# Performance work log

Hardware: AMD Instinct MI355X
Metric: run time of the kernel (lower is better)

Reference implementation:

```python
import jax, jax.numpy as jnp
import numpy as np

EPS = 1e-5

def layernorm(x):
    mu = jnp.mean(x, axis=-1, keepdims=True)
    var = jnp.var(x, axis=-1, keepdims=True)
    return (x - mu) * jax.lax.rsqrt(var + EPS)

def jagged_to_padded(values, offsets, n):
    # values: [T, D]; offsets: [B+1]; -> [B, n, D] zero-padded
    lengths = offsets[1:] - offsets[:-1]            # [B]
    pos = jnp.arange(n)                             # [n]
    idx = offsets[:-1, None] + pos[None, :]         # [B, n]
    mask = pos[None, :] < lengths[:, None]          # [B, n]
    idx = jnp.clip(idx, 0, values.shape[0] - 1)
    return values[idx] * mask[..., None].astype(values.dtype)

def dense_to_jagged(padded, offsets, total):
    t = jnp.arange(total)
    b = jnp.searchsorted(offsets, t, side='right') - 1   # row of each token
    p = t - offsets[b]                                   # position within row
    return padded[b, p]

def causal_conv(x, w, b):
    # x: [B, n, D]; w: [D, D, 3]; residual + bias + leaky_relu
    xt = jnp.transpose(x, (0, 2, 1))                     # [B, D, n]
    xt = jnp.pad(xt, ((0, 0), (0, 0), (2, 0)))           # causal left pad (k-1)
    y = jax.lax.conv_general_dilated(xt, w, (1,), 'VALID',
                                     dimension_numbers=('NCH', 'OIH', 'NCH'))
    y = y + b[None, :, None]
    y = jnp.transpose(y, (0, 2, 1)) + x                  # residual
    return jax.nn.leaky_relu(y, 0.01)

def setup_inputs() -> dict:
    key = jax.random.key(0)
    ks = jax.random.split(key, 8)
    B, n, D = 32, 4096, 256
    P, H, dA = 512, 8, 64
    T = B * (n // 2)  # equal lengths of 2048
    offsets = (jnp.arange(B + 1, dtype=jnp.int64 if jax.config.read('jax_enable_x64') else jnp.int32) * (n // 2)).astype(jnp.int32)
    return {
        'normed_x': jax.random.normal(ks[0], (T, D), dtype=jnp.float32),
        'conv_w': 0.02 * jax.random.normal(ks[1], (D, D, 3), dtype=jnp.float32),
        'conv_b': 0.02 * jax.random.normal(ks[2], (D,), dtype=jnp.float32),
        'pattern': 0.02 * jax.random.normal(ks[3], (P, D), dtype=jnp.float32),
        'wq': 0.02 * jax.random.normal(ks[4], (H * dA, D), dtype=jnp.float32),
        'wkv': 0.02 * jax.random.normal(ks[5], (2 * H * dA, D), dtype=jnp.float32),
        'wout': jax.random.uniform(ks[6], (D, H * dA), dtype=jnp.float32,
                                   minval=-1.0, maxval=1.0) * np.sqrt(6.0 / (D + H * dA)),
        'bout': jnp.zeros((D,), dtype=jnp.float32),
        'x_offsets': offsets,
        'n': n,
    }

def reference(normed_x, conv_w, conv_b, pattern, wq, wkv, wout, bout, x_offsets, n):
    H, dA = 8, 64
    scale = dA ** (-0.5)
    T = normed_x.shape[0]
    # jagged -> padded, causal conv (residual + leaky_relu), padded -> jagged
    padded = jagged_to_padded(normed_x, x_offsets, n)        # [B, n, D]
    padded = causal_conv(padded, conv_w, conv_b)
    x = dense_to_jagged(padded, x_offsets, T)                # [T, D]
    # pattern layernormed twice (SPRM.forward then xattn.forward)
    pat = layernorm(layernorm(pattern))                      # [P, D]
    x = layernorm(x)
    q = (x @ wq.T).reshape(T, H, dA)                         # [T, H, dA]
    kv = (pat @ wkv.T).reshape(pat.shape[0], H, 2 * dA)
    k, v = kv[..., :dA], kv[..., dA:]                        # [P, H, dA]
    scores = scale * jnp.einsum('nhd,whd->nhw', q, k)        # [T, H, P]
    attn = jax.nn.softmax(scores, axis=-1)
    out = jnp.einsum('nhw,whd->nhd', attn, v).reshape(T, H * dA)
    out = out @ wout.T + bout                                # [T, D]
    return layernorm(out)
```

## Files before the change

### kernel.cpp

```cpp
#include <hip/hip_runtime.h>
#include <hip/hip_bf16.h>
#include <math.h>


#define EPSF 1e-5f

typedef short  s16x8 __attribute__((ext_vector_type(8)));
typedef short  s16x4 __attribute__((ext_vector_type(4)));
typedef float  f32x4 __attribute__((ext_vector_type(4)));

__device__ __forceinline__ unsigned short f2bf(float f) {
    union { float f; unsigned u; } v; v.f = f;
    unsigned r = (v.u + 0x7fffu + ((v.u >> 16) & 1u)) >> 16;
    return (unsigned short)r;
}
__device__ __forceinline__ float bf2f(unsigned short h) {
    union { unsigned u; float f; } v; v.u = ((unsigned)h) << 16;
    return v.f;
}
__device__ __forceinline__ unsigned fbits(float f) {
    union { float f; unsigned u; } v; v.f = f; return v.u;
}
__device__ __forceinline__ unsigned pk_hi(float lo, float hi) {
    return __builtin_amdgcn_perm(fbits(hi), fbits(lo), 0x07060302u);
}
__device__ __forceinline__ int inv32(int t) {
    return (t & ~31) | ((t & 0x0C) << 1) | ((t & 0x10) >> 2) | (t & 3);
}

union Bfrag { unsigned u[4]; s16x8 s; };

__global__ void cvt_kernel(const float* __restrict__ wq,
                           const float* __restrict__ wout,
                           const float* __restrict__ cw,
                           short* __restrict__ wq_bf,
                           short* __restrict__ wout_bf,
                           short* __restrict__ wck) {
    const int b = blockIdx.x, tid = threadIdx.x;
    if (b < 128) {
        const int i = (b * 256 + tid) * 4;
        const int R = i >> 8, C = i & 255;
        const float4 x = *(const float4*)(wq + i);
        s16x4 o; o[0] = f2bf(x.x); o[1] = f2bf(x.y); o[2] = f2bf(x.z); o[3] = f2bf(x.w);
        const int off = ((R >> 6) * 32 + ((R >> 4) & 3) * 8 + (C >> 5)) * 512
                      + ((R & 15) + ((C >> 3) & 3) * 16) * 8 + (C & 7);
        *(s16x4*)(wq_bf + off) = o;
    } else if (b < 256) {
        const int i = ((b - 128) * 256 + tid) * 4;
        const float4 x = *(const float4*)(wout + i);
        s16x4 o; o[0] = f2bf(x.x); o[1] = f2bf(x.y); o[2] = f2bf(x.z); o[3] = f2bf(x.w);
        *(s16x4*)(wout_bf + i) = o;
    } else {
        const int idx = (b - 256) * 256 + tid;
        const float* p = cw + (size_t)idx * 3;
        wck[idx]              = (short)f2bf(p[0]);
        wck[65536 + idx]      = (short)f2bf(p[1]);
        wck[131072 + idx]     = (short)f2bf(p[2]);
    }
}

__global__ void pat_ln_kernel(const float* __restrict__ pattern,
                              float* __restrict__ pat2) {
    __shared__ float scr[4];
    const int w = blockIdx.x;
    const int tid = threadIdx.x;
    const int lane = tid & 63, wav = tid >> 6;

    float v = pattern[(size_t)w * 256 + tid];

    float s = v;
    #pragma unroll
    for (int off = 32; off; off >>= 1) s += __shfl_xor(s, off);
    if (lane == 0) scr[wav] = s;
    __syncthreads();
    float mu = (scr[0] + scr[1] + scr[2] + scr[3]) * (1.f / 256.f);
    __syncthreads();
    float d = v - mu;
    float s2 = d * d;
    #pragma unroll
    for (int off = 32; off; off >>= 1) s2 += __shfl_xor(s2, off);
    if (lane == 0) scr[wav] = s2;
    __syncthreads();
    float var = (scr[0] + scr[1] + scr[2] + scr[3]) * (1.f / 256.f);
    float x1 = d * rsqrtf(var + EPSF);
    __syncthreads();

    s = x1;
    #pragma unroll
    for (int off = 32; off; off >>= 1) s += __shfl_xor(s, off);
    if (lane == 0) scr[wav] = s;
    __syncthreads();
    mu = (scr[0] + scr[1] + scr[2] + scr[3]) * (1.f / 256.f);
    __syncthreads();
    d = x1 - mu;
    s2 = d * d;
    #pragma unroll
    for (int off = 32; off; off >>= 1) s2 += __shfl_xor(s2, off);
    if (lane == 0) scr[wav] = s2;
    __syncthreads();
    var = (scr[0] + scr[1] + scr[2] + scr[3]) * (1.f / 256.f);
    pat2[(size_t)w * 256 + tid] = d * rsqrtf(var + EPSF);
}

__global__ __launch_bounds__(256, 2)
void kv_frag_kernel(const float* __restrict__ pat2,
                    const float* __restrict__ wkv,
                    short* __restrict__ k_bf,
                    short* __restrict__ v_t) {
    __shared__ __align__(16) float spat[32][260];
    __shared__ __align__(16) float kvs[32][65];
    const int kt = blockIdx.x, h = blockIdx.y, z = blockIdx.z;
    const int t = threadIdx.x;

    {
        const int row = t >> 3;
        const float* src = pat2 + (size_t)(kt * 32 + row) * 256 + (t & 7) * 32;
        float* dst = &spat[row][(t & 7) * 32];
        #pragma unroll
        for (int q = 0; q < 8; q++)
            *(float4*)(dst + q * 4) = *(const float4*)(src + q * 4);
    }
    __syncthreads();

    {
        const int pr = t >> 3, rb = t & 7;
        const float* srow = &spat[pr][0];
        const float* wbase = wkv + (size_t)(h * 128 + z * 64 + rb) * 256;
        float acc[8] = {0.f, 0.f, 0.f, 0.f, 0.f, 0.f, 0.f, 0.f};
        for (int i4 = 0; i4 < 64; i4++) {
            const float4 x4 = *(const float4*)(srow + i4 * 4);
            #pragma unroll
            for (int i = 0; i < 8; i++) {
                const float4 w4 = *(const float4*)(wbase + (size_t)i * 8 * 256 + i4 * 4);
                acc[i] += w4.x * x4.x + w4.y * x4.y + w4.z * x4.z + w4.w * x4.w;
            }
        }
        #pragma unroll
        for (int i = 0; i < 8; i++)
            kvs[pr][rb + 8 * i] = acc[i];
    }
    __syncthreads();

    const int lane = t & 63;
    const int cl = lane & 15, gq = lane >> 4;
    if (z == 0) {
        const int f = t >> 6;
        const int pl = ((f >> 1) << 4) | cl;
        s16x8 o;
        #pragma unroll
        for (int e = 0; e < 8; e++) {
            const int c = (f & 1) * 32 + gq * 8 + e;
            const int r = (c & ~0x1C) | ((c & 0x18) >> 1) | ((c & 4) << 2);
            o[e] = (short)f2bf(kvs[pl][r] * 0.125f);
        }
        *(s16x8*)(k_bf + (size_t)h * 32768 + (size_t)kt * 2048 + t * 8) = o;
    } else {
        const int nd = t >> 6;
        const int rd = nd * 16 + cl;
        s16x8 o;
        #pragma unroll
        for (int e = 0; e < 8; e++) {
            const int c5 = gq * 8 + e;
            const int pl = (c5 & 3) | ((c5 & 0x18) >> 1) | ((c5 & 4) << 2);
            o[e] = (short)f2bf(kvs[pl][rd]);
        }
        *(s16x8*)(v_t + (size_t)h * 32768 + (size_t)kt * 2048 + t * 8) = o;
    }
}

__global__ __launch_bounds__(256, 4)
void conv_ln_kernel(const float* __restrict__ x,
                    const short* __restrict__ wck,
                    const float* __restrict__ cb,
                    short* __restrict__ xn_bf) {
    __shared__ __align__(16) short xs[66 * 268];
    const int tid = threadIdx.x;
    const int r0 = blockIdx.x * 64;
    const int pos0 = r0 & 2047;

    #pragma unroll
    for (int it = 0; it < 17; it++) {
        const int idx = tid + it * 256;
        if (idx < 4224) {
            const int row = idx >> 6, c4 = idx & 63;
            float4 v = {0.f, 0.f, 0.f, 0.f};
            if (pos0 - 2 + row >= 0)
                v = *(const float4*)(x + (size_t)(r0 - 2 + row) * 256 + c4 * 4);
            s16x4 o; o[0] = f2bf(v.x); o[1] = f2bf(v.y); o[2] = f2bf(v.z); o[3] = f2bf(v.w);
            *(s16x4*)(xs + row * 268 + c4 * 4) = o;
        }
    }
    __syncthreads();

    const int lane = tid & 63, w = tid >> 6, g = lane >> 4, cl = lane & 15;

    f32x4 acc[4][4];
    #pragma unroll
    for (int mt = 0; mt < 4; mt++)
        #pragma unroll
        for (int nt = 0; nt < 4; nt++) acc[mt][nt] = (f32x4){0.f, 0.f, 0.f, 0.f};

    #pragma unroll
    for (int kk = 0; kk < 3; kk++) {
        const short* wb = wck + kk * 65536;
        for (int s = 0; s < 8; s++) {
            s16x8 a[4];
            #pragma unroll
            for (int mt = 0; mt < 4; mt++)
                a[mt] = *(const s16x8*)(xs + (mt * 16 + cl + kk) * 268 + s * 32 + g * 8);
            #pragma unroll
            for (int nt = 0; nt < 4; nt++) {
                const s16x8 b = *(const s16x8*)(wb + (size_t)(w * 64 + nt * 16 + cl) * 256 + s * 32 + g * 8);
                #pragma unroll
                for (int mt = 0; mt < 4; mt++)
                    acc[mt][nt] = __builtin_amdgcn_mfma_f32_16x16x32_bf16(a[mt], b, acc[mt][nt], 0, 0, 0);
            }
        }
    }

    #pragma unroll
    for (int nt = 0; nt < 4; nt++) {
        const int col = w * 64 + nt * 16 + cl;
        const float b = cb[col];
        #pragma unroll
        for (int mt = 0; mt < 4; mt++)
            #pragma unroll
            for (int r = 0; r < 4; r++) {
                const int row = mt * 16 + g * 4 + r;
                float y = acc[mt][nt][r] + b + x[(size_t)(r0 + row) * 256 + col];
                acc[mt][nt][r] = (y >= 0.f) ? y : 0.01f * y;
            }
    }
    __syncthreads();
    #pragma unroll
    for (int mt = 0; mt < 4; mt++)
        #pragma unroll
        for (int nt = 0; nt < 4; nt++)
            #pragma unroll
            for (int r = 0; r < 4; r++)
                xs[(mt * 16 + g * 4 + r) * 268 + w * 64 + nt * 16 + cl] =
                    (short)f2bf(acc[mt][nt][r]);
    __syncthreads();

    for (int q = 0; q < 16; q++) {
        const int m = w * 16 + q;
        const s16x4 v4 = *(const s16x4*)(xs + m * 268 + lane * 4);
        const float f0 = bf2f((unsigned short)v4[0]), f1 = bf2f((unsigned short)v4[1]);
        const float f2 = bf2f((unsigned short)v4[2]), f3 = bf2f((unsigned short)v4[3]);
        float s = f0 + f1 + f2 + f3;
        #pragma unroll
        for (int off = 32; off; off >>= 1) s += __shfl_xor(s, off);
        const float mu = s * (1.f / 256.f);
        const float d0 = f0 - mu, d1 = f1 - mu, d2 = f2 - mu, d3 = f3 - mu;
        float vv = d0 * d0 + d1 * d1 + d2 * d2 + d3 * d3;
        #pragma unroll
        for (int off = 32; off; off >>= 1) vv += __shfl_xor(vv, off);
        const float rs = rsqrtf(vv * (1.f / 256.f) + EPSF);
        s16x4 o; o[0] = f2bf(d0 * rs); o[1] = f2bf(d1 * rs);
        o[2] = f2bf(d2 * rs); o[3] = f2bf(d3 * rs);
        *(s16x4*)(xn_bf + (size_t)(r0 + m) * 256 + lane * 4) = o;
    }
}

__global__ __launch_bounds__(256, 2)
void qattn_kernel(const short* __restrict__ xn_bf,
                  const short* __restrict__ wq_bf,
                  const short* __restrict__ k_bf,
                  const short* __restrict__ v_t,
                  short* __restrict__ ao_bf) {
    const int tid = threadIdx.x;
    const int lane = tid & 63, w = tid >> 6, g = lane >> 4, cl = lane & 15;
    const int q0 = blockIdx.x * 256 + w * 64 + cl;
    const int h0 = blockIdx.y * 2;
    const int fo = lane * 8;

    for (int hh = 0; hh < 2; ++hh) {
        const int h = h0 + hh;
        f32x4 qacc[4][4];
        #pragma unroll
        for (int u = 0; u < 4; u++)
            #pragma unroll
            for (int nt = 0; nt < 4; nt++) qacc[u][nt] = (f32x4){0.f, 0.f, 0.f, 0.f};
        for (int s = 0; s < 8; ++s) {
            s16x8 aw[4];
            #pragma unroll
            for (int nt = 0; nt < 4; ++nt)
                aw[nt] = *(const s16x8*)(wq_bf + ((size_t)(h * 4 + nt) * 8 + s) * 512 + fo);
            #pragma unroll
            for (int u = 0; u < 4; ++u) {
                const s16x8 bx = *(const s16x8*)(xn_bf + (size_t)(q0 + 16 * u) * 256 + s * 32 + g * 8);
                #pragma unroll
                for (int nt = 0; nt < 4; ++nt)
                    qacc[u][nt] = __builtin_amdgcn_mfma_f32_16x16x32_bf16(aw[nt], bx, qacc[u][nt], 0, 0, 0);
            }
        }
        Bfrag qB[4][2];
        #pragma unroll
        for (int u = 0; u < 4; ++u)
            #pragma unroll
            for (int s = 0; s < 2; ++s) {
                qB[u][s].u[0] = pk_hi(qacc[u][2 * s][0],     qacc[u][2 * s][1]);
                qB[u][s].u[1] = pk_hi(qacc[u][2 * s][2],     qacc[u][2 * s][3]);
                qB[u][s].u[2] = pk_hi(qacc[u][2 * s + 1][0], qacc[u][2 * s + 1][1]);
                qB[u][s].u[3] = pk_hi(qacc[u][2 * s + 1][2], qacc[u][2 * s + 1][3]);
            }

        float lsum[4] = {0.f, 0.f, 0.f, 0.f};
        f32x4 oacc[4][4];
        #pragma unroll
        for (int u = 0; u < 4; u++)
            #pragma unroll
            for (int nd = 0; nd < 4; nd++) oacc[u][nd] = (f32x4){0.f, 0.f, 0.f, 0.f};

        const short* kp = k_bf + (size_t)h * 32768;
        const short* vp = v_t  + (size_t)h * 32768;

        s16x8 kn0 = *(const s16x8*)(kp + fo);
        s16x8 kn1 = *(const s16x8*)(kp + fo + 512);
        s16x8 kn2 = *(const s16x8*)(kp + fo + 1024);
        s16x8 kn3 = *(const s16x8*)(kp + fo + 1536);

        for (int kt = 0; kt < 16; ++kt) {
            const s16x8 a00 = kn0, a01 = kn1, a10 = kn2, a11 = kn3;
            if (kt < 15) {
                const short* kn = kp + (kt + 1) * 2048 + fo;
                kn0 = *(const s16x8*)(kn);
                kn1 = *(const s16x8*)(kn + 512);
                kn2 = *(const s16x8*)(kn + 1024);
                kn3 = *(const s16x8*)(kn + 1536);
            }
            const short* vb = vp + kt * 2048 + fo;
            const s16x8 va0 = *(const s16x8*)(vb);
            const s16x8 va1 = *(const s16x8*)(vb + 512);
            const s16x8 va2 = *(const s16x8*)(vb + 1024);
            const s16x8 va3 = *(const s16x8*)(vb + 1536);

            f32x4 s0[4], s1[4];
            #pragma unroll
            for (int u = 0; u < 4; ++u) {
                s0[u] = (f32x4){0.f, 0.f, 0.f, 0.f};
                s1[u] = (f32x4){0.f, 0.f, 0.f, 0.f};
                s0[u] = __builtin_amdgcn_mfma_f32_16x16x32_bf16(a00, qB[u][0].s, s0[u], 0, 0, 0);
                s0[u] = __builtin_amdgcn_mfma_f32_16x16x32_bf16(a01, qB[u][1].s, s0[u], 0, 0, 0);
                s1[u] = __builtin_amdgcn_mfma_f32_16x16x32_bf16(a10, qB[u][0].s, s1[u], 0, 0, 0);
                s1[u] = __builtin_amdgcn_mfma_f32_16x16x32_bf16(a11, qB[u][1].s, s1[u], 0, 0, 0);
            }

            #pragma unroll
            for (int u = 0; u < 4; ++u)
                #pragma unroll
                for (int r = 0; r < 4; ++r) {
                    s0[u][r] = __expf(s0[u][r]); lsum[u] += s0[u][r];
                    s1[u][r] = __expf(s1[u][r]); lsum[u] += s1[u][r];
                }

            Bfrag pB[4];
            #pragma unroll
            for (int u = 0; u < 4; ++u) {
                pB[u].u[0] = pk_hi(s0[u][0], s0[u][1]);
                pB[u].u[1] = pk_hi(s0[u][2], s0[u][3]);
                pB[u].u[2] = pk_hi(s1[u][0], s1[u][1]);
                pB[u].u[3] = pk_hi(s1[u][2], s1[u][3]);
            }

            #pragma unroll
            for (int u = 0; u < 4; ++u) {
                oacc[u][0] = __builtin_amdgcn_mfma_f32_16x16x32_bf16(va0, pB[u].s, oacc[u][0], 0, 0, 0);
                oacc[u][1] = __builtin_amdgcn_mfma_f32_16x16x32_bf16(va1, pB[u].s, oacc[u][1], 0, 0, 0);
                oacc[u][2] = __builtin_amdgcn_mfma_f32_16x16x32_bf16(va2, pB[u].s, oacc[u][2], 0, 0, 0);
                oacc[u][3] = __builtin_amdgcn_mfma_f32_16x16x32_bf16(va3, pB[u].s, oacc[u][3], 0, 0, 0);
            }
        }

        #pragma unroll
        for (int u = 0; u < 4; ++u) {
            float s = lsum[u];
            s += __shfl_xor(s, 16);
            s += __shfl_xor(s, 32);
            const float inv = 1.f / s;
            const size_t qr = (size_t)(q0 + u * 16);
            #pragma unroll
            for (int nd = 0; nd < 4; ++nd) {
                const float o0 = oacc[u][nd][0] * inv, o1 = oacc[u][nd][1] * inv;
                const float o2 = oacc[u][nd][2] * inv, o3 = oacc[u][nd][3] * inv;
                const unsigned lo = (unsigned)f2bf(o0) | ((unsigned)f2bf(o1) << 16);
                const unsigned hi = (unsigned)f2bf(o2) | ((unsigned)f2bf(o3) << 16);
                short* dst = ao_bf + qr * 512 + h * 64 + nd * 16 + 4 * g;
                *(unsigned*)(dst)     = lo;
                *(unsigned*)(dst + 2) = hi;
            }
        }
    }
}

__global__ __launch_bounds__(256, 4)
void outproj_ln_kernel(const short* __restrict__ ao,
                       const short* __restrict__ wout_bf,
                       const float* __restrict__ bout,
                       float* __restrict__ out) {
    __shared__ __align__(16) char smem[33280];
    short* as = (short*)smem;
    float* ys = (float*)smem;
    const int tid = threadIdx.x;
    const int r0 = blockIdx.x * 32;

    #pragma unroll
    for (int it = 0; it < 8; it++) {
        const int idx = tid + it * 256;
        const int row = idx >> 6, c8 = idx & 63;
        const s16x8 v = *(const s16x8*)(ao + (size_t)(r0 + row) * 512 + c8 * 8);
        *(s16x8*)(as + row * 520 + c8 * 8) = v;
    }
    __syncthreads();

    const int lane = tid & 63, w = tid >> 6, g = lane >> 4, cl = lane & 15;

    f32x4 acc[2][4];
    #pragma unroll
    for (int mt = 0; mt < 2; mt++)
        #pragma unroll
        for (int nt = 0; nt < 4; nt++) acc[mt][nt] = (f32x4){0.f, 0.f, 0.f, 0.f};

    for (int s = 0; s < 16; s++) {
        const s16x8 a0 = *(const s16x8*)(as + cl * 520 + s * 32 + g * 8);
        const s16x8 a1 = *(const s16x8*)(as + (16 + cl) * 520 + s * 32 + g * 8);
        #pragma unroll
        for (int nt = 0; nt < 4; nt++) {
            const s16x8 b = *(const s16x8*)(wout_bf + (size_t)(w * 64 + nt * 16 + cl) * 512 + s * 32 + g * 8);
            acc[0][nt] = __builtin_amdgcn_mfma_f32_16x16x32_bf16(a0, b, acc[0][nt], 0, 0, 0);
            acc[1][nt] = __builtin_amdgcn_mfma_f32_16x16x32_bf16(a1, b, acc[1][nt], 0, 0, 0);
        }
    }
    __syncthreads();

    #pragma unroll
    for (int nt = 0; nt < 4; nt++) {
        const int col = w * 64 + nt * 16 + cl;
        const float b = bout[col];
        #pragma unroll
        for (int mt = 0; mt < 2; mt++)
            #pragma unroll
            for (int r = 0; r < 4; r++)
                ys[(mt * 16 + g * 4 + r) * 260 + col] = acc[mt][nt][r] + b;
    }
    __syncthreads();

    for (int q = 0; q < 8; q++) {
        const int m = w * 8 + q;
        const float4 v4 = *(const float4*)(ys + m * 260 + lane * 4);
        float s = v4.x + v4.y + v4.z + v4.w;
        #pragma unroll
        for (int off = 32; off; off >>= 1) s += __shfl_xor(s, off);
        const float mu = s * (1.f / 256.f);
        const float d0 = v4.x - mu, d1 = v4.y - mu, d2 = v4.z - mu, d3 = v4.w - mu;
        float vv = d0 * d0 + d1 * d1 + d2 * d2 + d3 * d3;
        #pragma unroll
        for (int off = 32; off; off >>= 1) vv += __shfl_xor(vv, off);
        const float rs = rsqrtf(vv * (1.f / 256.f) + EPSF);
        float4 o; o.x = d0 * rs; o.y = d1 * rs; o.z = d2 * rs; o.w = d3 * rs;
        *(float4*)(out + (size_t)(r0 + m) * 256 + lane * 4) = o;
    }
}

extern "C" void kernel_launch(void* const* d_in, const int* in_sizes, int n_in,
                              void* d_out, int out_size, void* d_ws, size_t ws_size,
                              hipStream_t stream) {
    const float* normed_x = (const float*)d_in[0];
    const float* conv_w   = (const float*)d_in[1];
    const float* conv_b   = (const float*)d_in[2];
    const float* pattern  = (const float*)d_in[3];
    const float* wq       = (const float*)d_in[4];
    const float* wkv      = (const float*)d_in[5];
    const float* wout     = (const float*)d_in[6];
    const float* bout     = (const float*)d_in[7];
    const int T = in_sizes[0] / 256;

    char* wsb = (char*)d_ws;
    short* xn_bf  = (short*)(wsb);
    short* ao_bf  = (short*)(wsb + (size_t)33554432);
    short* k_bf   = (short*)(wsb + (size_t)100663296);
    short* v_t    = (short*)(wsb + (size_t)101187584);
    short* wq_bf  = (short*)(wsb + (size_t)101711872);
    short* wout_bf= (short*)(wsb + (size_t)101974016);
    short* wck    = (short*)(wsb + (size_t)102236160);
    float* pat2   = (float*)(wsb + (size_t)33554432);
    float* out    = (float*)d_out;

    cvt_kernel<<<512, 256, 0, stream>>>(wq, wout, conv_w, wq_bf, wout_bf, wck);
    pat_ln_kernel<<<512, 256, 0, stream>>>(pattern, pat2);
    kv_frag_kernel<<<dim3(16, 8, 2), 256, 0, stream>>>(pat2, wkv, k_bf, v_t);
    conv_ln_kernel<<<T / 64, 256, 0, stream>>>(normed_x, wck, conv_b, xn_bf);
    qattn_kernel<<<dim3(T / 256, 4), 256, 0, stream>>>(xn_bf, wq_bf, k_bf, v_t, ao_bf);
    outproj_ln_kernel<<<T / 32, 256, 0, stream>>>(ao_bf, wout_bf, bout, out);
}
```

Baseline: 474.2 us.

## Pre-swizzle weights and attention output into MFMA fragment layout; use exp2 softmax

The conv and out-projection weights are now written in a fragment-tiled layout, so each lane loads its B fragment as one contiguous 16-byte read. The attention output is written directly in A-fragment tile order, which lets the out-projection kernel drop its shared-memory staging and one barrier and read fragments straight from global memory. K is pre-scaled by scale·log2(e) so the softmax can use exp2 instead of exp. In exchange, the out-projection A operand now comes from global/L2 on every k step instead of from LDS.

```diff
diff --git a/kernel.cpp b/kernel.cpp
--- a/kernel.cpp
+++ b/kernel.cpp
@@ -4,6 +4,7 @@
 
 
 #define EPSF 1e-5f
+#define KSCALE 0.18033688f
 
 typedef short  s16x8 __attribute__((ext_vector_type(8)));
 typedef short  s16x4 __attribute__((ext_vector_type(4)));
@@ -23,9 +24,6 @@
 }
 __device__ __forceinline__ unsigned pk_hi(float lo, float hi) {
     return __builtin_amdgcn_perm(fbits(hi), fbits(lo), 0x07060302u);
-}
-__device__ __forceinline__ int inv32(int t) {
-    return (t & ~31) | ((t & 0x0C) << 1) | ((t & 0x10) >> 2) | (t & 3);
 }
 
 union Bfrag { unsigned u[4]; s16x8 s; };
@@ -47,15 +45,21 @@
         *(s16x4*)(wq_bf + off) = o;
     } else if (b < 256) {
         const int i = ((b - 128) * 256 + tid) * 4;
+        const int R = i >> 9, C = i & 511;
         const float4 x = *(const float4*)(wout + i);
         s16x4 o; o[0] = f2bf(x.x); o[1] = f2bf(x.y); o[2] = f2bf(x.z); o[3] = f2bf(x.w);
-        *(s16x4*)(wout_bf + i) = o;
+        const int off = ((R >> 4) * 16 + (C >> 5)) * 512
+                      + ((R & 15) + ((C >> 3) & 3) * 16) * 8 + (C & 7);
+        *(s16x4*)(wout_bf + off) = o;
     } else {
         const int idx = (b - 256) * 256 + tid;
+        const int o = idx >> 8, i = idx & 255;
         const float* p = cw + (size_t)idx * 3;
-        wck[idx]              = (short)f2bf(p[0]);
-        wck[65536 + idx]      = (short)f2bf(p[1]);
-        wck[131072 + idx]     = (short)f2bf(p[2]);
+        const int off = ((o >> 4) * 8 + (i >> 5)) * 512
+                      + ((o & 15) + ((i >> 3) & 3) * 16) * 8 + (i & 7);
+        wck[off]           = (short)f2bf(p[0]);
+        wck[65536 + off]   = (short)f2bf(p[1]);
+        wck[131072 + off]  = (short)f2bf(p[2]);
     }
 }
 
@@ -151,7 +155,7 @@
         for (int e = 0; e < 8; e++) {
             const int c = (f & 1) * 32 + gq * 8 + e;
             const int r = (c & ~0x1C) | ((c & 0x18) >> 1) | ((c & 4) << 2);
-            o[e] = (short)f2bf(kvs[pl][r] * 0.125f);
+            o[e] = (short)f2bf(kvs[pl][r] * KSCALE);
         }
         *(s16x8*)(k_bf + (size_t)h * 32768 + (size_t)kt * 2048 + t * 8) = o;
     } else {
@@ -193,6 +197,7 @@
     __syncthreads();
 
     const int lane = tid & 63, w = tid >> 6, g = lane >> 4, cl = lane & 15;
+    const int fo = lane * 8;
 
     f32x4 acc[4][4];
     #pragma unroll
@@ -210,7 +215,7 @@
                 a[mt] = *(const s16x8*)(xs + (mt * 16 + cl + kk) * 268 + s * 32 + g * 8);
             #pragma unroll
             for (int nt = 0; nt < 4; nt++) {
-                const s16x8 b = *(const s16x8*)(wb + (size_t)(w * 64 + nt * 16 + cl) * 256 + s * 32 + g * 8);
+                const s16x8 b = *(const s16x8*)(wb + ((w * 4 + nt) * 8 + s) * 512 + fo);
                 #pragma unroll
                 for (int mt = 0; mt < 4; mt++)
                     acc[mt][nt] = __builtin_amdgcn_mfma_f32_16x16x32_bf16(a[mt], b, acc[mt][nt], 0, 0, 0);
@@ -271,6 +276,7 @@
     const int tid = threadIdx.x;
     const int lane = tid & 63, w = tid >> 6, g = lane >> 4, cl = lane & 15;
     const int q0 = blockIdx.x * 256 + w * 64 + cl;
+    const int rt0 = blockIdx.x * 16 + w * 4;
     const int h0 = blockIdx.y * 2;
     const int fo = lane * 8;
 
@@ -350,8 +356,8 @@
             for (int u = 0; u < 4; ++u)
                 #pragma unroll
                 for (int r = 0; r < 4; ++r) {
-                    s0[u][r] = __expf(s0[u][r]); lsum[u] += s0[u][r];
-                    s1[u][r] = __expf(s1[u][r]); lsum[u] += s1[u][r];
+                    s0[u][r] = __builtin_exp2f(s0[u][r]); lsum[u] += s0[u][r];
+                    s1[u][r] = __builtin_exp2f(s1[u][r]); lsum[u] += s1[u][r];
                 }
 
             Bfrag pB[4];
@@ -378,14 +384,15 @@
             s += __shfl_xor(s, 16);
             s += __shfl_xor(s, 32);
             const float inv = 1.f / s;
-            const size_t qr = (size_t)(q0 + u * 16);
             #pragma unroll
             for (int nd = 0; nd < 4; ++nd) {
                 const float o0 = oacc[u][nd][0] * inv, o1 = oacc[u][nd][1] * inv;
                 const float o2 = oacc[u][nd][2] * inv, o3 = oacc[u][nd][3] * inv;
                 const unsigned lo = (unsigned)f2bf(o0) | ((unsigned)f2bf(o1) << 16);
                 const unsigned hi = (unsigned)f2bf(o2) | ((unsigned)f2bf(o3) << 16);
-                short* dst = ao_bf + qr * 512 + h * 64 + nd * 16 + 4 * g;
+                short* dst = ao_bf
+                    + ((size_t)(rt0 + u) * 16 + (h * 2 + (nd >> 1))) * 512
+                    + (cl + 16 * ((nd * 2 + (g >> 1)) & 3)) * 8 + (g & 1) * 4;
                 *(unsigned*)(dst)     = lo;
                 *(unsigned*)(dst + 2) = hi;
             }
@@ -398,22 +405,11 @@
                        const short* __restrict__ wout_bf,
                        const float* __restrict__ bout,
                        float* __restrict__ out) {
-    __shared__ __align__(16) char smem[33280];
-    short* as = (short*)smem;
-    float* ys = (float*)smem;
+    __shared__ __align__(16) float ys[32 * 260];
     const int tid = threadIdx.x;
     const int r0 = blockIdx.x * 32;
-
-    #pragma unroll
-    for (int it = 0; it < 8; it++) {
-        const int idx = tid + it * 256;
-        const int row = idx >> 6, c8 = idx & 63;
-        const s16x8 v = *(const s16x8*)(ao + (size_t)(r0 + row) * 512 + c8 * 8);
-        *(s16x8*)(as + row * 520 + c8 * 8) = v;
-    }
-    __syncthreads();
-
     const int lane = tid & 63, w = tid >> 6, g = lane >> 4, cl = lane & 15;
+    const int fo = lane * 8;
 
     f32x4 acc[2][4];
     #pragma unroll
@@ -421,12 +417,14 @@
         #pragma unroll
         for (int nt = 0; nt < 4; nt++) acc[mt][nt] = (f32x4){0.f, 0.f, 0.f, 0.f};
 
+    const short* af = ao + (size_t)(blockIdx.x * 2) * 16 * 512;
+
     for (int s = 0; s < 16; s++) {
-        const s16x8 a0 = *(const s16x8*)(as + cl * 520 + s * 32 + g * 8);
-        const s16x8 a1 = *(const s16x8*)(as + (16 + cl) * 520 + s * 32 + g * 8);
+        const s16x8 a0 = *(const s16x8*)(af + (size_t)s * 512 + fo);
+        const s16x8 a1 = *(const s16x8*)(af + (size_t)(16 + s) * 512 + fo);
         #pragma unroll
         for (int nt = 0; nt < 4; nt++) {
-            const s16x8 b = *(const s16x8*)(wout_bf + (size_t)(w * 64 + nt * 16 + cl) * 512 + s * 32 + g * 8);
+            const s16x8 b = *(const s16x8*)(wout_bf + (size_t)((w * 4 + nt) * 16 + s) * 512 + fo);
             acc[0][nt] = __builtin_amdgcn_mfma_f32_16x16x32_bf16(a0, b, acc[0][nt], 0, 0, 0);
             acc[1][nt] = __builtin_amdgcn_mfma_f32_16x16x32_bf16(a1, b, acc[1][nt], 0, 0, 0);
         }
```

After: 462.1 us. 2.6% less time.
